# Kernel optimization log

Measured on AMD Instinct MI355X. Metric: run time of the kernel, lower is better.

Reference implementation:

```python
import jax, jax.numpy as jnp
import numpy as np

EPS = 1e-5

def _subsys_level(x, W, b, g, beta):
    # x: [S,B,I], W: [S,O,I]  -> Linear -> Tanh -> BatchNorm(batch stats over B)
    h = jnp.einsum('sbi,soi->sbo', x, W) + b[:, None, :]
    h = jnp.tanh(h)
    mu = jnp.mean(h, axis=1, keepdims=True)
    var = jnp.var(h, axis=1, keepdims=True)
    return g[:, None, :] * (h - mu) * jax.lax.rsqrt(var + EPS) + beta[:, None, :]

def setup_inputs() -> dict:
    key = jax.random.key(0)
    ks = jax.random.split(key, 16)
    B, N = 4096, 6000
    u = lambda k, shp: jax.random.uniform(k, shp, jnp.float32, -0.001, 0.001)
    return {
        'mutant_state': jax.random.uniform(ks[0], (B, N), jnp.float32),
        'gene_idx': jax.random.randint(ks[1], (512, 16), 0, N),
        'W1': u(ks[2], (512, 20, 16)), 'b1': u(ks[3], (512, 20)),
        'g1': jnp.ones((512, 20), jnp.float32), 'beta1': jnp.zeros((512, 20), jnp.float32),
        'W2': u(ks[4], (64, 24, 160)), 'b2': u(ks[5], (64, 24)),
        'g2': jnp.ones((64, 24), jnp.float32), 'beta2': jnp.zeros((64, 24), jnp.float32),
        'W3': u(ks[6], (8, 32, 192)), 'b3': u(ks[7], (8, 32)),
        'g3': jnp.ones((8, 32), jnp.float32), 'beta3': jnp.zeros((8, 32), jnp.float32),
        'Wr': u(ks[8], (64, 256)), 'br': u(ks[9], (64,)),
        'gr': jnp.ones((64,), jnp.float32), 'betar': jnp.zeros((64,), jnp.float32),
    }

def reference(mutant_state, gene_idx, W1, b1, g1, beta1, W2, b2, g2, beta2,
              W3, b3, g3, beta3, Wr, br, gr, betar):
    B = mutant_state.shape[0]
    # Level 1 (leaves): gather per-term gene mutant states -> [S1,B,G]
    x1 = jnp.transpose(mutant_state[:, gene_idx], (1, 0, 2))  # [512,B,16]
    o1 = _subsys_level(x1, W1, b1, g1, beta1)                  # [512,B,20]
    # Level 2: each of 64 parents concatenates 8 children outputs -> [64,B,160]
    x2 = o1.reshape(64, 8, B, 20).transpose(0, 2, 1, 3).reshape(64, B, 160)
    o2 = _subsys_level(x2, W2, b2, g2, beta2)                  # [64,B,24]
    # Level 3: 8 parents x 8 children -> [8,B,192]
    x3 = o2.reshape(8, 8, B, 24).transpose(0, 2, 1, 3).reshape(8, B, 192)
    o3 = _subsys_level(x3, W3, b3, g3, beta3)                  # [8,B,32]
    # Root: concat 8 outputs -> [B,256]
    xr = o3.transpose(1, 0, 2).reshape(B, 256)
    hr = jnp.tanh(xr @ Wr.T + br)
    mu = jnp.mean(hr, axis=0, keepdims=True)
    var = jnp.var(hr, axis=0, keepdims=True)
    return gr * (hr - mu) * jax.lax.rsqrt(var + EPS) + betar  # [B,64]
```

## Files before the change

kernel.cpp:

```cpp
#include <hip/hip_runtime.h>
#include <hip/hip_fp16.h>

#define BATCH 4096
#define EPS 1e-5f

typedef __half h16;
typedef float f32x2 __attribute__((ext_vector_type(2)));
typedef float f32x4 __attribute__((ext_vector_type(4)));
typedef _Float16 half8 __attribute__((ext_vector_type(8)));
typedef unsigned int u32;

union H8 { float4 f4; h16 h[8]; __half2 h2[4]; };
union U4 { float4 f4; u32 u[4]; };
union H2U { float f; __half2 h2; u32 u; };
union FRU { uint4 q; half8 h; };

__device__ __forceinline__ float tanh_fast(float x){
  float e = __expf(2.0f*x);
  return 1.0f - 2.0f*__builtin_amdgcn_rcpf(e + 1.0f);
}

__device__ __forceinline__ float wred(float v){
  #pragma unroll
  for (int off=32; off; off>>=1) v += __shfl_xor(v, off);
  return v;
}

__global__ __launch_bounds__(256) void k_transpose(const float* __restrict__ ms, h16* __restrict__ msT){
  __shared__ float tile[64][65];
  int tc = blockIdx.x * 64;
  int tb = blockIdx.y * 64;
  int tx = threadIdx.x & 63;
  int ty = threadIdx.x >> 6;
  #pragma unroll
  for (int k=0;k<16;++k){
    int r = ty + k*4;
    int c = tc + tx;
    if (c < 6000) tile[r][tx] = ms[(size_t)(tb + r)*6000 + c];
  }
  __syncthreads();
  #pragma unroll
  for (int k=0;k<16;++k){
    int r = ty + k*4;
    int c = tc + r;
    if (c < 6000) msT[(size_t)c*BATCH + tb + tx] = __float2half(tile[tx][r]);
  }
}

__global__ __launch_bounds__(64,2) void k_statsA(const h16* __restrict__ msT, const int* __restrict__ gidx,
    const float* __restrict__ W1, const float* __restrict__ b1,
    u32* __restrict__ H1p, float* __restrict__ part1){
  const int s = blockIdx.y;
  const int bc = blockIdx.x;
  const int lane = threadIdx.x;
  const int b0 = bc*512 + lane*8;
  const float* Wp = W1 + s*320;
  f32x2 acc[20][4];
  #pragma unroll
  for (int o=0;o<20;++o){
    float bv = b1[s*20+o];
    #pragma unroll
    for (int k=0;k<4;++k) acc[o][k] = (f32x2){bv,bv};
  }
  #pragma unroll 4
  for (int g=0; g<16; ++g){
    const int row = gidx[s*16+g]*BATCH;
    H8 u; u.f4 = *reinterpret_cast<const float4*>(msT + row + b0);
    f32x2 x[4];
    #pragma unroll
    for (int k=0;k<4;++k){
      float2 f = __half22float2(u.h2[k]);
      x[k] = (f32x2){f.x, f.y};
    }
    #pragma unroll
    for (int o=0;o<20;++o){
      float wv = Wp[o*16+g];
      f32x2 w2 = (f32x2){wv,wv};
      #pragma unroll
      for (int k=0;k<4;++k) acc[o][k] = __builtin_elementwise_fma(x[k], w2, acc[o][k]);
    }
  }
  #pragma unroll
  for (int op=0;op<10;++op){
    const int oA = 2*op, oB = 2*op+1;
    float hA[8], hB[8];
    #pragma unroll
    for (int k=0;k<4;++k){
      hA[2*k]   = tanh_fast(acc[oA][k].x);
      hA[2*k+1] = tanh_fast(acc[oA][k].y);
      hB[2*k]   = tanh_fast(acc[oB][k].x);
      hB[2*k+1] = tanh_fast(acc[oB][k].y);
    }
    U4 v0, v1;
    #pragma unroll
    for (int k=0;k<4;++k){
      H2U a; a.h2 = __halves2half2(__float2half(hA[k]),   __float2half(hB[k]));   v0.u[k] = a.u;
      H2U b; b.h2 = __halves2half2(__float2half(hA[k+4]), __float2half(hB[k+4])); v1.u[k] = b.u;
    }
    u32* dst = H1p + (size_t)(s*10+op)*BATCH + b0;
    *reinterpret_cast<float4*>(dst)     = v0.f4;
    *reinterpret_cast<float4*>(dst + 4) = v1.f4;
    float SA = ((hA[0]+hA[1])+(hA[2]+hA[3])) + ((hA[4]+hA[5])+(hA[6]+hA[7]));
    float QA = ((hA[0]*hA[0]+hA[1]*hA[1])+(hA[2]*hA[2]+hA[3]*hA[3]))
             + ((hA[4]*hA[4]+hA[5]*hA[5])+(hA[6]*hA[6]+hA[7]*hA[7]));
    float SB = ((hB[0]+hB[1])+(hB[2]+hB[3])) + ((hB[4]+hB[5])+(hB[6]+hB[7]));
    float QB = ((hB[0]*hB[0]+hB[1]*hB[1])+(hB[2]*hB[2]+hB[3]*hB[3]))
             + ((hB[4]*hB[4]+hB[5]*hB[5])+(hB[6]*hB[6]+hB[7]*hB[7]));
    SA = wred(SA); QA = wred(QA); SB = wred(SB); QB = wred(QB);
    if (lane==0){
      part1[((s*20+oA)*2  )*8 + bc] = SA;
      part1[((s*20+oA)*2+1)*8 + bc] = QA;
      part1[((s*20+oB)*2  )*8 + bc] = SB;
      part1[((s*20+oB)*2+1)*8 + bc] = QB;
    }
  }
}

__global__ __launch_bounds__(256) void k_fold2(const float* __restrict__ W, const float* __restrict__ bb,
    const float* __restrict__ g, const float* __restrict__ beta,
    const float* __restrict__ part, uint4* __restrict__ Wfrag, float* __restrict__ bf){
  const int p = blockIdx.x;
  const int tid = threadIdx.x;
  __shared__ float aL[160], cL[160];
  for (int t = tid; t < 160; t += 256){
    int ch = p*160 + t;
    float S=0.f, Q=0.f;
    for (int bc=0; bc<8; ++bc){ S += part[(ch*2)*8 + bc]; Q += part[(ch*2+1)*8 + bc]; }
    float mu  = S * (1.0f/BATCH);
    float var = Q * (1.0f/BATCH) - mu*mu;
    float a = g[ch] * rsqrtf(var + EPS);
    aL[t] = a;
    cL[t] = beta[ch] - a*mu;
  }
  __syncthreads();
  for (int E = tid; E < 640; E += 256){
    int f = E >> 6, l = E & 63;
    int jt = f/5, kc = f%5;
    int j = jt*16 + (l&15);
    int gg = l>>4;
    u32 q[4];
    #pragma unroll
    for (int e2=0; e2<4; ++e2){
      int i0 = kc*32 + gg*8 + 2*e2;
      float w0=0.f, w1=0.f;
      if (j < 24){
        w0 = W[p*3840 + j*160 + i0    ] * aL[i0];
        w1 = W[p*3840 + j*160 + i0 + 1] * aL[i0+1];
      }
      H2U u; u.h2 = __halves2half2(__float2half(w0), __float2half(w1));
      q[e2] = u.u;
    }
    Wfrag[p*640 + E] = make_uint4(q[0],q[1],q[2],q[3]);
  }
  if (tid < 24){
    float sv = bb[p*24 + tid];
    for (int i=0;i<160;++i) sv = fmaf(W[p*3840 + tid*160 + i], cL[i], sv);
    bf[p*24 + tid] = sv;
  }
}

__global__ __launch_bounds__(256) void k_passB(const u32* __restrict__ H1p,
    const uint4* __restrict__ Wfrag, const float* __restrict__ b2f,
    h16* __restrict__ H2){
  const int p = blockIdx.y;
  const int bc = blockIdx.x;
  const int tid = threadIdx.x;
  const int wv = tid >> 6;
  const int l = tid & 63;
  const int g = l >> 4;
  __shared__ u32 lds[64*84];
  half8 wf[10];
  #pragma unroll
  for (int f=0; f<10; ++f){
    FRU u; u.q = Wfrag[p*640 + f*64 + l];
    wf[f] = u.h;
  }
  const u32* __restrict__ hp = H1p + (size_t)p*80*BATCH;
  const float* bp = b2f + p*24;
  float bj0[4], bj1[4];
  #pragma unroll
  for (int r=0;r<4;++r){
    bj0[r] = bp[g*4+r];
    bj1[r] = (g<2) ? bp[16+g*4+r] : 0.f;
  }
  for (int it=0; it<4; ++it){
    const int b0 = bc*256 + it*64;
    __syncthreads();
    #pragma unroll
    for (int rr=0; rr<20; ++rr){
      int r = rr*4 + wv;
      lds[l*84 + r] = hp[(size_t)r*BATCH + b0 + l];
    }
    __syncthreads();
    const int bb = wv*16 + (l&15);
    f32x4 acc0 = {0.f,0.f,0.f,0.f}, acc1 = {0.f,0.f,0.f,0.f};
    #pragma unroll
    for (int kc=0; kc<5; ++kc){
      FRU u; u.q = *reinterpret_cast<const uint4*>(&lds[bb*84 + kc*16 + g*4]);
      acc0 = __builtin_amdgcn_mfma_f32_16x16x32_f16(wf[kc],   u.h, acc0, 0,0,0);
      acc1 = __builtin_amdgcn_mfma_f32_16x16x32_f16(wf[5+kc], u.h, acc1, 0,0,0);
    }
    const int B = b0 + bb;
    h16* dst = H2 + ((size_t)p*BATCH + B)*24;
    {
      H2U u0,u1;
      u0.h2 = __halves2half2(__float2half(tanh_fast(acc0[0]+bj0[0])), __float2half(tanh_fast(acc0[1]+bj0[1])));
      u1.h2 = __halves2half2(__float2half(tanh_fast(acc0[2]+bj0[2])), __float2half(tanh_fast(acc0[3]+bj0[3])));
      *reinterpret_cast<uint2*>(dst + g*4) = make_uint2(u0.u, u1.u);
    }
    if (g < 2){
      H2U u0,u1;
      u0.h2 = __halves2half2(__float2half(tanh_fast(acc1[0]+bj1[0])), __float2half(tanh_fast(acc1[1]+bj1[1])));
      u1.h2 = __halves2half2(__float2half(tanh_fast(acc1[2]+bj1[2])), __float2half(tanh_fast(acc1[3]+bj1[3])));
      *reinterpret_cast<uint2*>(dst + 16 + g*4) = make_uint2(u0.u, u1.u);
    }
  }
}

__global__ __launch_bounds__(256) void k_stats2(const h16* __restrict__ H2, float* __restrict__ part2){
  const int p = blockIdx.y;
  const int bc = blockIdx.x;
  const int tid = threadIdx.x;
  const int wv = tid >> 6;
  const int lane = tid & 63;
  float S[24], Q[24];
  #pragma unroll
  for (int j=0;j<24;++j){ S[j]=0.f; Q[j]=0.f; }
  const h16* base = H2 + ((size_t)p*BATCH + bc*1024 + tid)*24;
  for (int it=0; it<4; ++it){
    const h16* src = base + (size_t)it*256*24;
    #pragma unroll
    for (int t=0;t<3;++t){
      H8 u; u.f4 = *reinterpret_cast<const float4*>(src + t*8);
      #pragma unroll
      for (int i=0;i<8;++i){
        float v = __half2float(u.h[i]);
        S[t*8+i] += v;
        Q[t*8+i] = fmaf(v, v, Q[t*8+i]);
      }
    }
  }
  __shared__ float red[2][4][24];
  #pragma unroll
  for (int j=0;j<24;++j){
    float s = wred(S[j]);
    float q = wred(Q[j]);
    if (lane==0){ red[0][wv][j] = s; red[1][wv][j] = q; }
  }
  __syncthreads();
  if (tid < 24){
    float s = (red[0][0][tid]+red[0][1][tid]) + (red[0][2][tid]+red[0][3][tid]);
    float q = (red[1][0][tid]+red[1][1][tid]) + (red[1][2][tid]+red[1][3][tid]);
    const int ch = p*24 + tid;
    part2[(ch*2  )*4 + bc] = s;
    part2[(ch*2+1)*4 + bc] = q;
  }
}

__global__ __launch_bounds__(512) void k_passC(const h16* __restrict__ H2, const float* __restrict__ part2,
    const float* __restrict__ g2, const float* __restrict__ beta2,
    const float* __restrict__ W3, const float* __restrict__ b3,
    h16* __restrict__ H3, float* __restrict__ part3){
  const int q = blockIdx.y;
  const int bc = blockIdx.x;
  const int tid = threadIdx.x;
  const int wv = tid >> 6;
  const int lane = tid & 63;
  __shared__ float aL[192], cL[192];
  for (int t = tid; t < 192; t += 512){
    int ch = q*192 + t;
    float S=0.f, Q=0.f;
    #pragma unroll
    for (int c=0;c<4;++c){ S += part2[(ch*2)*4 + c]; Q += part2[(ch*2+1)*4 + c]; }
    float mu  = S * (1.0f/BATCH);
    float var = Q * (1.0f/BATCH) - mu*mu;
    float a = g2[ch] * rsqrtf(var + EPS);
    aL[t] = a; cL[t] = beta2[ch] - a*mu;
  }
  __syncthreads();
  const int b = bc*64 + lane;
  const int jb = wv*4;
  float acc[4];
  #pragma unroll
  for (int j=0;j<4;++j) acc[j] = b3[q*32 + jb + j];
  for (int c2=0;c2<8;++c2){
    const h16* src = H2 + ((size_t)(q*8+c2)*BATCH + b)*24;
    float xn[24];
    #pragma unroll
    for (int t=0;t<3;++t){
      H8 u; u.f4 = *reinterpret_cast<const float4*>(src + t*8);
      #pragma unroll
      for (int i=0;i<8;++i){
        int ci = c2*24 + t*8 + i;
        xn[t*8+i] = fmaf(aL[ci], __half2float(u.h[i]), cL[ci]);
      }
    }
    #pragma unroll
    for (int j=0;j<4;++j){
      const float* wr = W3 + q*6144 + (jb+j)*192 + c2*24;
      #pragma unroll
      for (int i=0;i<24;++i) acc[j] = fmaf(xn[i], wr[i], acc[j]);
    }
  }
  #pragma unroll
  for (int j=0;j<4;++j) acc[j] = tanh_fast(acc[j]);
  {
    h16* dst = H3 + (size_t)b*256 + q*32 + jb;
    H2U u0,u1;
    u0.h2 = __halves2half2(__float2half(acc[0]), __float2half(acc[1]));
    u1.h2 = __halves2half2(__float2half(acc[2]), __float2half(acc[3]));
    float2 vv; vv.x = u0.f; vv.y = u1.f;
    *reinterpret_cast<float2*>(dst) = vv;
  }
  #pragma unroll
  for (int j=0;j<4;++j){
    float S = wred(acc[j]);
    float Q = wred(acc[j]*acc[j]);
    if (lane==0){
      part3[((q*32+jb+j)*2  )*64 + bc] = S;
      part3[((q*32+jb+j)*2+1)*64 + bc] = Q;
    }
  }
}

__global__ __launch_bounds__(256) void k_passD(const h16* __restrict__ H3, const float* __restrict__ part3,
    const float* __restrict__ g3, const float* __restrict__ beta3,
    const float* __restrict__ Wr, const float* __restrict__ br,
    float* __restrict__ Hr, float* __restrict__ partR){
  const int bc = blockIdx.x;
  const int jb = blockIdx.y * 8;
  const int tid = threadIdx.x;
  const int wv = tid >> 6;
  const int lane = tid & 63;
  __shared__ float aL[256], cL[256];
  __shared__ float lacc[4][64][9];
  {
    float S=0.f, Q=0.f;
    for (int c=0;c<64;++c){ S += part3[(tid*2)*64 + c]; Q += part3[(tid*2+1)*64 + c]; }
    float mu  = S * (1.0f/BATCH);
    float var = Q * (1.0f/BATCH) - mu*mu;
    float a = g3[tid] * rsqrtf(var + EPS);
    aL[tid] = a; cL[tid] = beta3[tid] - a*mu;
  }
  __syncthreads();
  const int b = bc*64 + lane;
  float acc[8];
  #pragma unroll
  for (int j=0;j<8;++j) acc[j] = 0.f;
  const h16* src = H3 + (size_t)b*256 + wv*64;
  #pragma unroll
  for (int kk=0; kk<8; ++kk){
    const int sl = wv*8 + kk;
    H8 u; u.f4 = *reinterpret_cast<const float4*>(src + kk*8);
    float xn[8];
    #pragma unroll
    for (int i=0;i<8;++i){
      int ci = sl*8+i;
      xn[i] = fmaf(aL[ci], __half2float(u.h[i]), cL[ci]);
    }
    #pragma unroll
    for (int j=0;j<8;++j){
      const float* wr = Wr + (jb+j)*256 + sl*8;
      #pragma unroll
      for (int i=0;i<8;++i) acc[j] = fmaf(xn[i], wr[i], acc[j]);
    }
  }
  #pragma unroll
  for (int j=0;j<8;++j) lacc[wv][lane][j] = acc[j];
  __syncthreads();
  #pragma unroll
  for (int k=0;k<2;++k){
    const int j = k*4 + wv;
    float v = br[jb+j] + (lacc[0][lane][j] + lacc[1][lane][j]) + (lacc[2][lane][j] + lacc[3][lane][j]);
    v = tanh_fast(v);
    Hr[(size_t)b*64 + jb + j] = v;
    float S = wred(v);
    float Q = wred(v*v);
    if (lane==0){
      partR[((jb+j)*2  )*64 + bc] = S;
      partR[((jb+j)*2+1)*64 + bc] = Q;
    }
  }
}

__global__ __launch_bounds__(256) void k_final(const float* __restrict__ Hr, const float* __restrict__ partR,
    const float* __restrict__ gr, const float* __restrict__ betar, float* __restrict__ out){
  __shared__ float aL[64], cL[64];
  const int tid = threadIdx.x;
  if (tid < 64){
    float S=0.f, Q=0.f;
    for (int bc=0; bc<64; ++bc){ S += partR[(tid*2)*64 + bc]; Q += partR[(tid*2+1)*64 + bc]; }
    float mu  = S * (1.0f/BATCH);
    float var = Q * (1.0f/BATCH) - mu*mu;
    float a = gr[tid] * rsqrtf(var + EPS);
    aL[tid] = a; cL[tid] = betar[tid] - a*mu;
  }
  __syncthreads();
  const int i4 = blockIdx.x*256 + tid;
  float4 v = *reinterpret_cast<const float4*>(Hr + (size_t)i4*4);
  int o = (i4*4)&63;
  float4 r;
  r.x = aL[o  ]*v.x + cL[o  ];
  r.y = aL[o+1]*v.y + cL[o+1];
  r.z = aL[o+2]*v.z + cL[o+2];
  r.w = aL[o+3]*v.w + cL[o+3];
  *reinterpret_cast<float4*>(out + (size_t)i4*4) = r;
}

extern "C" void kernel_launch(void* const* d_in, const int* in_sizes, int n_in,
                              void* d_out, int out_size, void* d_ws, size_t ws_size,
                              hipStream_t stream) {
  const float* ms    = (const float*)d_in[0];
  const int*   gidx  = (const int*)  d_in[1];
  const float* W1    = (const float*)d_in[2];
  const float* b1    = (const float*)d_in[3];
  const float* g1    = (const float*)d_in[4];
  const float* beta1 = (const float*)d_in[5];
  const float* W2    = (const float*)d_in[6];
  const float* b2    = (const float*)d_in[7];
  const float* g2    = (const float*)d_in[8];
  const float* beta2 = (const float*)d_in[9];
  const float* W3    = (const float*)d_in[10];
  const float* b3    = (const float*)d_in[11];
  const float* g3    = (const float*)d_in[12];
  const float* beta3 = (const float*)d_in[13];
  const float* Wr    = (const float*)d_in[14];
  const float* br    = (const float*)d_in[15];
  const float* gr    = (const float*)d_in[16];
  const float* betar = (const float*)d_in[17];
  float* out = (float*)d_out;

  char* w = (char*)d_ws;
  size_t off = 0;
  auto take = [&](size_t bytes)->char*{
    char* p = w + off;
    off = (off + bytes + 255) & ~(size_t)255;
    return p;
  };
  h16*   msT    = (h16*)  take((size_t)6000*BATCH*2);
  u32*   H1p    = (u32*)  take((size_t)5120*BATCH*4);
  h16*   H2     = (h16*)  take((size_t)64*BATCH*24*2);
  h16*   H3     = (h16*)  take((size_t)BATCH*256*2);
  float* Hr     = (float*)take((size_t)BATCH*64*4);
  float* part1  = (float*)take((size_t)10240*2*8*4);
  float* part2  = (float*)take((size_t)1536*2*4*4);
  float* part3  = (float*)take((size_t)256*2*64*4);
  float* partR  = (float*)take((size_t)64*2*64*4);
  uint4* Wfrag  = (uint4*)take((size_t)64*640*16);
  float* b2f    = (float*)take((size_t)64*24*4);
  if (off > ws_size) return;

  k_transpose<<<dim3(94,64), 256, 0, stream>>>(ms, msT);
  k_statsA<<<dim3(8,512), 64, 0, stream>>>(msT, gidx, W1, b1, H1p, part1);
  k_fold2<<<64, 256, 0, stream>>>(W2, b2, g1, beta1, part1, Wfrag, b2f);
  k_passB<<<dim3(16,64), 256, 0, stream>>>(H1p, Wfrag, b2f, H2);
  k_stats2<<<dim3(4,64), 256, 0, stream>>>(H2, part2);
  k_passC<<<dim3(64,8), 512, 0, stream>>>(H2, part2, g2, beta2, W3, b3, H3, part3);
  k_passD<<<dim3(64,8), 256, 0, stream>>>(H3, part3, g3, beta3, Wr, br, Hr, partR);
  k_final<<<256, 256, 0, stream>>>(Hr, partR, gr, betar, out);
}
```

Measured before the change: 155.9 us.

## Compute level-1 subsystem linear layer with MFMA f16 instead of scalar FMA

Rewrites the leaf-level kernel to stage gathered gene rows in LDS and compute the 16->20 projection with 16x16x32 f16 MFMA instructions. Weights are converted to half fragments, and the grid doubles to 16 batch chunks of 256. Per-channel partial sums for batch statistics now go to 16 slots, and the fold kernel and workspace are adjusted to match. The aim is to cut VALU FMA work and register pressure, at the cost of half-precision weights, MFMAs that are half-idle (K=16 zero-padded to 32, only 20 of 32 output rows used), and narrower 4-byte scattered stores.

```diff
diff --git a/kernel.cpp b/kernel.cpp
--- a/kernel.cpp
+++ b/kernel.cpp
@@ -9,11 +9,12 @@
 typedef float f32x4 __attribute__((ext_vector_type(4)));
 typedef _Float16 half8 __attribute__((ext_vector_type(8)));
 typedef unsigned int u32;
+typedef unsigned short u16;
 
 union H8 { float4 f4; h16 h[8]; __half2 h2[4]; };
-union U4 { float4 f4; u32 u[4]; };
 union H2U { float f; __half2 h2; u32 u; };
 union FRU { uint4 q; half8 h; };
+union FRU8 { u16 us[8]; half8 h; };
 
 __device__ __forceinline__ float tanh_fast(float x){
   float e = __expf(2.0f*x);
@@ -47,71 +48,117 @@
   }
 }
 
-__global__ __launch_bounds__(64,2) void k_statsA(const h16* __restrict__ msT, const int* __restrict__ gidx,
+__global__ __launch_bounds__(64) void k_statsA(const h16* __restrict__ msT, const int* __restrict__ gidx,
     const float* __restrict__ W1, const float* __restrict__ b1,
     u32* __restrict__ H1p, float* __restrict__ part1){
-  const int s = blockIdx.y;
+  const int s  = blockIdx.y;
   const int bc = blockIdx.x;
-  const int lane = threadIdx.x;
-  const int b0 = bc*512 + lane*8;
-  const float* Wp = W1 + s*320;
-  f32x2 acc[20][4];
-  #pragma unroll
-  for (int o=0;o<20;++o){
-    float bv = b1[s*20+o];
-    #pragma unroll
-    for (int k=0;k<4;++k) acc[o][k] = (f32x2){bv,bv};
-  }
-  #pragma unroll 4
+  const int l  = threadIdx.x;
+  const int g4 = l >> 4;
+  const int lc = l & 15;
+  const int b0 = bc*256;
+  __shared__ u16 xls[16][260];
+
+  half8 wf0 = {}, wf1 = {};
+  if (g4 < 2){
+    {
+      const float* wp = W1 + s*320 + lc*16 + g4*8;
+      float4 wa = *reinterpret_cast<const float4*>(wp);
+      float4 wb = *reinterpret_cast<const float4*>(wp+4);
+      wf0[0]=(_Float16)wa.x; wf0[1]=(_Float16)wa.y; wf0[2]=(_Float16)wa.z; wf0[3]=(_Float16)wa.w;
+      wf0[4]=(_Float16)wb.x; wf0[5]=(_Float16)wb.y; wf0[6]=(_Float16)wb.z; wf0[7]=(_Float16)wb.w;
+    }
+    if (lc < 4){
+      const float* wp = W1 + s*320 + (16+lc)*16 + g4*8;
+      float4 wa = *reinterpret_cast<const float4*>(wp);
+      float4 wb = *reinterpret_cast<const float4*>(wp+4);
+      wf1[0]=(_Float16)wa.x; wf1[1]=(_Float16)wa.y; wf1[2]=(_Float16)wa.z; wf1[3]=(_Float16)wa.w;
+      wf1[4]=(_Float16)wb.x; wf1[5]=(_Float16)wb.y; wf1[6]=(_Float16)wb.z; wf1[7]=(_Float16)wb.w;
+    }
+  }
+  float bj0[4], bj1[4];
+  #pragma unroll
+  for (int r=0;r<4;++r){
+    bj0[r] = b1[s*20 + g4*4 + r];
+    bj1[r] = (g4==0) ? b1[s*20 + 16 + r] : 0.f;
+  }
+  #pragma unroll
   for (int g=0; g<16; ++g){
     const int row = gidx[s*16+g]*BATCH;
-    H8 u; u.f4 = *reinterpret_cast<const float4*>(msT + row + b0);
-    f32x2 x[4];
-    #pragma unroll
-    for (int k=0;k<4;++k){
-      float2 f = __half22float2(u.h2[k]);
-      x[k] = (f32x2){f.x, f.y};
-    }
-    #pragma unroll
-    for (int o=0;o<20;++o){
-      float wv = Wp[o*16+g];
-      f32x2 w2 = (f32x2){wv,wv};
+    float2 v = *reinterpret_cast<const float2*>(msT + row + b0 + l*4);
+    *reinterpret_cast<float2*>(&xls[g][l*4]) = v;
+  }
+  __syncthreads();
+
+  float S[8], Q[8];
+  #pragma unroll
+  for (int k=0;k<8;++k){ S[k]=0.f; Q[k]=0.f; }
+
+  for (int bt=0; bt<16; ++bt){
+    const int b = bt*16 + lc;
+    half8 xb = {};
+    if (g4 < 2){
+      FRU8 u;
       #pragma unroll
-      for (int k=0;k<4;++k) acc[o][k] = __builtin_elementwise_fma(x[k], w2, acc[o][k]);
-    }
-  }
-  #pragma unroll
-  for (int op=0;op<10;++op){
-    const int oA = 2*op, oB = 2*op+1;
-    float hA[8], hB[8];
-    #pragma unroll
-    for (int k=0;k<4;++k){
-      hA[2*k]   = tanh_fast(acc[oA][k].x);
-      hA[2*k+1] = tanh_fast(acc[oA][k].y);
-      hB[2*k]   = tanh_fast(acc[oB][k].x);
-      hB[2*k+1] = tanh_fast(acc[oB][k].y);
-    }
-    U4 v0, v1;
-    #pragma unroll
-    for (int k=0;k<4;++k){
-      H2U a; a.h2 = __halves2half2(__float2half(hA[k]),   __float2half(hB[k]));   v0.u[k] = a.u;
-      H2U b; b.h2 = __halves2half2(__float2half(hA[k+4]), __float2half(hB[k+4])); v1.u[k] = b.u;
-    }
-    u32* dst = H1p + (size_t)(s*10+op)*BATCH + b0;
-    *reinterpret_cast<float4*>(dst)     = v0.f4;
-    *reinterpret_cast<float4*>(dst + 4) = v1.f4;
-    float SA = ((hA[0]+hA[1])+(hA[2]+hA[3])) + ((hA[4]+hA[5])+(hA[6]+hA[7]));
-    float QA = ((hA[0]*hA[0]+hA[1]*hA[1])+(hA[2]*hA[2]+hA[3]*hA[3]))
-             + ((hA[4]*hA[4]+hA[5]*hA[5])+(hA[6]*hA[6]+hA[7]*hA[7]));
-    float SB = ((hB[0]+hB[1])+(hB[2]+hB[3])) + ((hB[4]+hB[5])+(hB[6]+hB[7]));
-    float QB = ((hB[0]*hB[0]+hB[1]*hB[1])+(hB[2]*hB[2]+hB[3]*hB[3]))
-             + ((hB[4]*hB[4]+hB[5]*hB[5])+(hB[6]*hB[6]+hB[7]*hB[7]));
-    SA = wred(SA); QA = wred(QA); SB = wred(SB); QB = wred(QB);
-    if (lane==0){
-      part1[((s*20+oA)*2  )*8 + bc] = SA;
-      part1[((s*20+oA)*2+1)*8 + bc] = QA;
-      part1[((s*20+oB)*2  )*8 + bc] = SB;
-      part1[((s*20+oB)*2+1)*8 + bc] = QB;
+      for (int e=0;e<8;++e) u.us[e] = xls[g4*8+e][b];
+      xb = u.h;
+    }
+    f32x4 z = {0.f,0.f,0.f,0.f};
+    f32x4 c0 = __builtin_amdgcn_mfma_f32_16x16x32_f16(wf0, xb, z, 0,0,0);
+    f32x4 c1 = __builtin_amdgcn_mfma_f32_16x16x32_f16(wf1, xb, z, 0,0,0);
+    const size_t bofs = (size_t)(b0 + bt*16 + lc);
+    {
+      float h0 = tanh_fast(c0[0]+bj0[0]);
+      float h1 = tanh_fast(c0[1]+bj0[1]);
+      float h2 = tanh_fast(c0[2]+bj0[2]);
+      float h3 = tanh_fast(c0[3]+bj0[3]);
+      S[0]+=h0; Q[0]=fmaf(h0,h0,Q[0]);
+      S[1]+=h1; Q[1]=fmaf(h1,h1,Q[1]);
+      S[2]+=h2; Q[2]=fmaf(h2,h2,Q[2]);
+      S[3]+=h3; Q[3]=fmaf(h3,h3,Q[3]);
+      H2U p0; p0.h2 = __halves2half2(__float2half(h0), __float2half(h1));
+      H2U p1; p1.h2 = __halves2half2(__float2half(h2), __float2half(h3));
+      const int op0 = g4*2;
+      H1p[(size_t)(s*10+op0  )*BATCH + bofs] = p0.u;
+      H1p[(size_t)(s*10+op0+1)*BATCH + bofs] = p1.u;
+    }
+    if (g4 == 0){
+      float h0 = tanh_fast(c1[0]+bj1[0]);
+      float h1 = tanh_fast(c1[1]+bj1[1]);
+      float h2 = tanh_fast(c1[2]+bj1[2]);
+      float h3 = tanh_fast(c1[3]+bj1[3]);
+      S[4]+=h0; Q[4]=fmaf(h0,h0,Q[4]);
+      S[5]+=h1; Q[5]=fmaf(h1,h1,Q[5]);
+      S[6]+=h2; Q[6]=fmaf(h2,h2,Q[6]);
+      S[7]+=h3; Q[7]=fmaf(h3,h3,Q[7]);
+      H2U p0; p0.h2 = __halves2half2(__float2half(h0), __float2half(h1));
+      H2U p1; p1.h2 = __halves2half2(__float2half(h2), __float2half(h3));
+      H1p[(size_t)(s*10+8)*BATCH + bofs] = p0.u;
+      H1p[(size_t)(s*10+9)*BATCH + bofs] = p1.u;
+    }
+  }
+  #pragma unroll
+  for (int k=0;k<8;++k){
+    #pragma unroll
+    for (int off=1; off<16; off<<=1){
+      S[k] += __shfl_xor(S[k], off);
+      Q[k] += __shfl_xor(Q[k], off);
+    }
+  }
+  if (lc == 0){
+    #pragma unroll
+    for (int r=0;r<4;++r){
+      int ch = s*20 + g4*4 + r;
+      part1[(ch*2  )*16 + bc] = S[r];
+      part1[(ch*2+1)*16 + bc] = Q[r];
+    }
+    if (g4 == 0){
+      #pragma unroll
+      for (int r=0;r<4;++r){
+        int ch = s*20 + 16 + r;
+        part1[(ch*2  )*16 + bc] = S[4+r];
+        part1[(ch*2+1)*16 + bc] = Q[4+r];
+      }
     }
   }
 }
@@ -125,7 +172,7 @@
   for (int t = tid; t < 160; t += 256){
     int ch = p*160 + t;
     float S=0.f, Q=0.f;
-    for (int bc=0; bc<8; ++bc){ S += part[(ch*2)*8 + bc]; Q += part[(ch*2+1)*8 + bc]; }
+    for (int bc=0; bc<16; ++bc){ S += part[(ch*2)*16 + bc]; Q += part[(ch*2+1)*16 + bc]; }
     float mu  = S * (1.0f/BATCH);
     float var = Q * (1.0f/BATCH) - mu*mu;
     float a = g[ch] * rsqrtf(var + EPS);
@@ -442,7 +489,7 @@
   h16*   H2     = (h16*)  take((size_t)64*BATCH*24*2);
   h16*   H3     = (h16*)  take((size_t)BATCH*256*2);
   float* Hr     = (float*)take((size_t)BATCH*64*4);
-  float* part1  = (float*)take((size_t)10240*2*8*4);
+  float* part1  = (float*)take((size_t)10240*2*16*4);
   float* part2  = (float*)take((size_t)1536*2*4*4);
   float* part3  = (float*)take((size_t)256*2*64*4);
   float* partR  = (float*)take((size_t)64*2*64*4);
@@ -451,7 +498,7 @@
   if (off > ws_size) return;
 
   k_transpose<<<dim3(94,64), 256, 0, stream>>>(ms, msT);
-  k_statsA<<<dim3(8,512), 64, 0, stream>>>(msT, gidx, W1, b1, H1p, part1);
+  k_statsA<<<dim3(16,512), 64, 0, stream>>>(msT, gidx, W1, b1, H1p, part1);
   k_fold2<<<64, 256, 0, stream>>>(W2, b2, g1, beta1, part1, Wfrag, b2f);
   k_passB<<<dim3(16,64), 256, 0, stream>>>(H1p, Wfrag, b2f, H2);
   k_stats2<<<dim3(4,64), 256, 0, stream>>>(H2, part2);
```

Result: no change. 157.8 us (+1.2%).
